# Performance work log

Hardware: AMD Instinct MI355X
Metric: run time of the kernel (lower is better)

Reference implementation:

```python
import jax, jax.numpy as jnp
import numpy as np

B, S, D, H, E, K = 4, 2048, 1024, 4096, 8, 2


def setup_inputs() -> dict:
    key = jax.random.key(0)
    ks = jax.random.split(key, 8)
    scale = 0.02
    x = jax.random.normal(ks[0], (B, S, D), dtype=jnp.float32)
    gate_w = jax.random.normal(ks[1], (D, E), dtype=jnp.float32) * scale
    gate_b = jnp.zeros((E,), dtype=jnp.float32)
    w1 = jax.random.normal(ks[2], (E, D, H), dtype=jnp.float32) * scale
    b1 = jnp.zeros((E, H), dtype=jnp.float32)
    w2 = jax.random.normal(ks[3], (E, H, D), dtype=jnp.float32) * scale
    b2 = jnp.zeros((E, D), dtype=jnp.float32)
    return {"x": x, "gate_w": gate_w, "gate_b": gate_b,
            "w1": w1, "b1": b1, "w2": w2, "b2": b2}


def reference(x, gate_w, gate_b, w1, b1, w2, b2):
    b, s, d = x.shape
    xf = x.reshape(-1, d)                              # [T, D]
    T = xf.shape[0]
    gates = xf @ gate_w + gate_b                       # [T, E]
    scores, idx = jax.lax.top_k(gates, K)              # [T, K] each
    g = jax.nn.softmax(scores, axis=-1)                # softmax over top-k slots
    # Per-token, per-expert combine weight (top-k indices are distinct)
    Wte = jnp.zeros((T, E), dtype=xf.dtype).at[jnp.arange(T)[:, None], idx].add(g)
    # Loop over the small fixed expert set via scan, accumulating weighted outputs.
    def body(acc, p):
        w1e, b1e, w2e, b2e, we = p                     # we: [T]
        h = jax.nn.gelu(xf @ w1e + b1e, approximate=False)  # [T, H]
        y = h @ w2e + b2e                              # [T, D]
        return acc + we[:, None] * y, None
    out, _ = jax.lax.scan(body, jnp.zeros_like(xf), (w1, b1, w2, b2, Wte.T))
    return out.reshape(b, s, d)
```

## Files before the change

kernel.cpp:

```cpp
#include <hip/hip_runtime.h>
#include <hip/hip_bf16.h>

#define Bb 4
#define Ss 2048
#define Dd 1024
#define Hh 4096
#define Ee 8
#define Tt (Bb*Ss)

typedef __attribute__((ext_vector_type(8))) short short8;
typedef __attribute__((ext_vector_type(4))) float floatx4;
typedef unsigned short u16;
typedef unsigned int u32;

__device__ __forceinline__ u16 f2bf(float f) {
  union { float f; u32 u; } v; v.f = f;
  return (u16)((v.u + 0x7FFFu + ((v.u >> 16) & 1u)) >> 16);
}

__device__ __forceinline__ void async16(const u16* g, u16* l) {
  __builtin_amdgcn_global_load_lds(
      (const __attribute__((address_space(1))) unsigned int*)g,
      (__attribute__((address_space(3))) unsigned int*)l, 16, 0, 0);
}

__global__ __launch_bounds__(256) void cvt_x(const float* __restrict__ x, u16* __restrict__ xb) {
  size_t i = ((size_t)blockIdx.x * 256 + threadIdx.x) * 8;
  float4 a = *(const float4*)(x + i);
  float4 b = *(const float4*)(x + i + 4);
  union { u16 us[8]; uint4 v; } o;
  o.us[0] = f2bf(a.x); o.us[1] = f2bf(a.y); o.us[2] = f2bf(a.z); o.us[3] = f2bf(a.w);
  o.us[4] = f2bf(b.x); o.us[5] = f2bf(b.y); o.us[6] = f2bf(b.z); o.us[7] = f2bf(b.w);
  *(uint4*)(xb + i) = o.v;
}

__global__ __launch_bounds__(256) void tconv(const float* __restrict__ src, u16* __restrict__ dst,
                                             int R, int C) {
  __shared__ float tile[64][65];
  int e = blockIdx.z;
  int r0 = blockIdx.y * 64, c0 = blockIdx.x * 64;
  int tx = threadIdx.x & 63, ty = threadIdx.x >> 6;
  const float* s = src + (size_t)e * R * C;
  u16* d = dst + (size_t)e * R * C;
#pragma unroll
  for (int i = 0; i < 16; i++) {
    int r = i * 4 + ty;
    tile[r][tx] = s[(size_t)(r0 + r) * C + c0 + tx];
  }
  __syncthreads();
#pragma unroll
  for (int i = 0; i < 16; i++) {
    int c = i * 4 + ty;
    d[(size_t)(c0 + c) * R + r0 + tx] = f2bf(tile[tx][c]);
  }
}

__global__ __launch_bounds__(256) void gate_kernel(const float* __restrict__ x,
                                                   const float* __restrict__ gw,
                                                   const float* __restrict__ gb,
                                                   int* __restrict__ counts,
                                                   int* __restrict__ tokL,
                                                   int* __restrict__ pairL,
                                                   float* __restrict__ wtL) {
  __shared__ float gwl[Dd * Ee];
  for (int i = threadIdx.x; i < Dd * Ee; i += 256) gwl[i] = gw[i];
  __syncthreads();
  int wid = threadIdx.x >> 6, lane = threadIdx.x & 63;
  int t = blockIdx.x * 4 + wid;
  const float* xr = x + (size_t)t * Dd;
  double acc[Ee];
#pragma unroll
  for (int e = 0; e < Ee; e++) acc[e] = 0.0;
  for (int i = 0; i < Dd / 64; i++) {
    int d = lane + i * 64;
    float xv = xr[d];
#pragma unroll
    for (int e = 0; e < Ee; e++) acc[e] += (double)xv * (double)gwl[d * Ee + e];
  }
#pragma unroll
  for (int off = 32; off > 0; off >>= 1)
#pragma unroll
    for (int e = 0; e < Ee; e++) acc[e] += __shfl_down(acc[e], off);
  if (lane == 0) {
    float s[Ee];
#pragma unroll
    for (int e = 0; e < Ee; e++) s[e] = (float)acc[e] + gb[e];
    int i0 = 0;
#pragma unroll
    for (int e = 1; e < Ee; e++) if (s[e] > s[i0]) i0 = e;
    int i1 = (i0 == 0) ? 1 : 0;
#pragma unroll
    for (int e = 0; e < Ee; e++) if (e != i0 && s[e] > s[i1]) i1 = e;
    float ex = expf(s[i1] - s[i0]);
    float g0 = 1.0f / (1.0f + ex);
    float g1 = ex / (1.0f + ex);
    int p0 = atomicAdd(&counts[i0], 1);
    tokL[i0 * Tt + p0] = t; pairL[i0 * Tt + p0] = t * 2;     wtL[i0 * Tt + p0] = g0;
    int p1 = atomicAdd(&counts[i1], 1);
    tokL[i1 * Tt + p1] = t; pairL[i1 * Tt + p1] = t * 2 + 1; wtL[i1 * Tt + p1] = g1;
  }
}

__global__ __launch_bounds__(256) void gemm1(const u16* __restrict__ xb,
                                             const u16* __restrict__ w1t,
                                             const float* __restrict__ b1,
                                             const int* __restrict__ counts,
                                             const int* __restrict__ tokL,
                                             const int* __restrict__ pairL,
                                             u16* __restrict__ h) {
  const int NT = 32;
  int e = blockIdx.z;
  int cnt = counts[e];
  int flat = blockIdx.x + NT * blockIdx.y;
  int x8 = flat & 7, j = flat >> 3;
  int n_t = j % NT;
  int m_t = (j / NT) * 8 + x8;
  int m0 = m_t * 128;
  if (m0 >= cnt) return;
  int rows = cnt - m0; if (rows > 128) rows = 128;
  int n0 = n_t * 128;

  __shared__ __align__(16) u16 As[2 * 128 * 32];
  __shared__ __align__(16) u16 Bs[2 * 128 * 32];
  __shared__ int ltok[128];
  __shared__ int lpair[128];

  int tid = threadIdx.x;
  if (tid < 128) {
    int ok = tid < rows;
    ltok[tid]  = ok ? tokL[e * Tt + m0 + tid] : tokL[e * Tt + m0];
    lpair[tid] = ok ? pairL[e * Tt + m0 + tid] : 0;
  }
  __syncthreads();

  int wv = tid >> 6, ln = tid & 63;
  int half = wv & 1;
  const u16* gp[4];
  u16* ldst[4];
  if (wv < 2) {
#pragma unroll
    for (int q = 0; q < 4; q++) {
      int r = half * 64 + q * 16 + (ln >> 2);
      int c = (ln & 3) ^ ((r >> 1) & 3);
      gp[q] = xb + (size_t)ltok[r] * Dd + c * 8;
      ldst[q] = As + (half * 64 + q * 16) * 32;
    }
  } else {
#pragma unroll
    for (int q = 0; q < 4; q++) {
      int r = half * 64 + q * 16 + (ln >> 2);
      int c = (ln & 3) ^ ((r >> 1) & 3);
      gp[q] = w1t + ((size_t)e * Hh + n0 + r) * Dd + c * 8;
      ldst[q] = Bs + (half * 64 + q * 16) * 32;
    }
  }

  floatx4 zero4 = {0.f, 0.f, 0.f, 0.f};
  floatx4 acc[4][4];
#pragma unroll
  for (int i = 0; i < 4; i++)
#pragma unroll
    for (int jj = 0; jj < 4; jj++) acc[i][jj] = zero4;

  int wr = wv >> 1, wc = wv & 1;
  int lm = ln & 15, lq = ln >> 4;

  const int NK = Dd / 32;
#pragma unroll
  for (int q = 0; q < 4; q++) async16(gp[q], ldst[q]);
#pragma unroll
  for (int q = 0; q < 4; q++) gp[q] += 32;

  for (int it = 0; it < NK; ++it) {
    if (it + 1 < NK) {
      int nb = (it + 1) & 1;
#pragma unroll
      for (int q = 0; q < 4; q++) async16(gp[q], ldst[q] + nb * 4096);
#pragma unroll
      for (int q = 0; q < 4; q++) gp[q] += 32;
      asm volatile("s_waitcnt vmcnt(4)" ::: "memory");
    } else {
      asm volatile("s_waitcnt vmcnt(0)" ::: "memory");
    }
    __builtin_amdgcn_s_barrier();
    int cb = it & 1;
    const u16* Ab = As + cb * 4096;
    const u16* Bp = Bs + cb * 4096;
    short8 a[4], b[4];
#pragma unroll
    for (int i = 0; i < 4; i++) {
      int row = wr * 64 + i * 16 + lm;
      int p = lq ^ ((row >> 1) & 3);
      a[i] = *(const short8*)(Ab + row * 32 + p * 8);
    }
#pragma unroll
    for (int jj = 0; jj < 4; jj++) {
      int row = wc * 64 + jj * 16 + lm;
      int p = lq ^ ((row >> 1) & 3);
      b[jj] = *(const short8*)(Bp + row * 32 + p * 8);
    }
#pragma unroll
    for (int i = 0; i < 4; i++)
#pragma unroll
      for (int jj = 0; jj < 4; jj++)
        acc[i][jj] = __builtin_amdgcn_mfma_f32_16x16x32_bf16(a[i], b[jj], acc[i][jj], 0, 0, 0);
    asm volatile("s_waitcnt lgkmcnt(0)" ::: "memory");
    __builtin_amdgcn_s_barrier();
  }

#pragma unroll
  for (int i = 0; i < 4; i++) {
    int rbase = wr * 64 + i * 16 + lq * 4;
#pragma unroll
    for (int r = 0; r < 4; r++) {
      int row = rbase + r;
      if (row < rows) {
        int p = lpair[row];
#pragma unroll
        for (int jj = 0; jj < 4; jj++) {
          int col = n0 + wc * 64 + jj * 16 + lm;
          float v = acc[i][jj][r] + b1[e * Hh + col];
          v = 0.5f * v * (1.0f + erff(v * 0.70710678118f));
          h[(size_t)p * Hh + col] = f2bf(v);
        }
      }
    }
  }
}

__global__ __launch_bounds__(256) void gemm2(const u16* __restrict__ h,
                                             const u16* __restrict__ w2t,
                                             const float* __restrict__ b2,
                                             const int* __restrict__ counts,
                                             const int* __restrict__ tokL,
                                             const int* __restrict__ pairL,
                                             const float* __restrict__ wtL,
                                             float* __restrict__ out) {
  const int NT = 8;
  int e = blockIdx.z;
  int cnt = counts[e];
  int flat = blockIdx.x + NT * blockIdx.y;
  int x8 = flat & 7, j = flat >> 3;
  int n_t = j % NT;
  int m_t = (j / NT) * 8 + x8;
  int m0 = m_t * 128;
  if (m0 >= cnt) return;
  int rows = cnt - m0; if (rows > 128) rows = 128;
  int n0 = n_t * 128;

  __shared__ __align__(16) u16 As[2 * 128 * 32];
  __shared__ __align__(16) u16 Bs[2 * 128 * 32];
  __shared__ int ltok[128];
  __shared__ int lpair[128];
  __shared__ float lwt[128];

  int tid = threadIdx.x;
  if (tid < 128) {
    int ok = tid < rows;
    ltok[tid]  = ok ? tokL[e * Tt + m0 + tid] : 0;
    lpair[tid] = ok ? pairL[e * Tt + m0 + tid] : pairL[e * Tt + m0];
    lwt[tid]   = ok ? wtL[e * Tt + m0 + tid] : 0.f;
  }
  __syncthreads();

  int wv = tid >> 6, ln = tid & 63;
  int half = wv & 1;
  const u16* gp[4];
  u16* ldst[4];
  if (wv < 2) {
#pragma unroll
    for (int q = 0; q < 4; q++) {
      int r = half * 64 + q * 16 + (ln >> 2);
      int c = (ln & 3) ^ ((r >> 1) & 3);
      gp[q] = h + (size_t)lpair[r] * Hh + c * 8;
      ldst[q] = As + (half * 64 + q * 16) * 32;
    }
  } else {
#pragma unroll
    for (int q = 0; q < 4; q++) {
      int r = half * 64 + q * 16 + (ln >> 2);
      int c = (ln & 3) ^ ((r >> 1) & 3);
      gp[q] = w2t + ((size_t)e * Dd + n0 + r) * Hh + c * 8;
      ldst[q] = Bs + (half * 64 + q * 16) * 32;
    }
  }

  floatx4 zero4 = {0.f, 0.f, 0.f, 0.f};
  floatx4 acc[4][4];
#pragma unroll
  for (int i = 0; i < 4; i++)
#pragma unroll
    for (int jj = 0; jj < 4; jj++) acc[i][jj] = zero4;

  int wr = wv >> 1, wc = wv & 1;
  int lm = ln & 15, lq = ln >> 4;

  const int NK = Hh / 32;
#pragma unroll
  for (int q = 0; q < 4; q++) async16(gp[q], ldst[q]);
#pragma unroll
  for (int q = 0; q < 4; q++) gp[q] += 32;

  for (int it = 0; it < NK; ++it) {
    if (it + 1 < NK) {
      int nb = (it + 1) & 1;
#pragma unroll
      for (int q = 0; q < 4; q++) async16(gp[q], ldst[q] + nb * 4096);
#pragma unroll
      for (int q = 0; q < 4; q++) gp[q] += 32;
      asm volatile("s_waitcnt vmcnt(4)" ::: "memory");
    } else {
      asm volatile("s_waitcnt vmcnt(0)" ::: "memory");
    }
    __builtin_amdgcn_s_barrier();
    int cb = it & 1;
    const u16* Ab = As + cb * 4096;
    const u16* Bp = Bs + cb * 4096;
    short8 a[4], b[4];
#pragma unroll
    for (int i = 0; i < 4; i++) {
      int row = wr * 64 + i * 16 + lm;
      int p = lq ^ ((row >> 1) & 3);
      a[i] = *(const short8*)(Ab + row * 32 + p * 8);
    }
#pragma unroll
    for (int jj = 0; jj < 4; jj++) {
      int row = wc * 64 + jj * 16 + lm;
      int p = lq ^ ((row >> 1) & 3);
      b[jj] = *(const short8*)(Bp + row * 32 + p * 8);
    }
#pragma unroll
    for (int i = 0; i < 4; i++)
#pragma unroll
      for (int jj = 0; jj < 4; jj++)
        acc[i][jj] = __builtin_amdgcn_mfma_f32_16x16x32_bf16(a[i], b[jj], acc[i][jj], 0, 0, 0);
    asm volatile("s_waitcnt lgkmcnt(0)" ::: "memory");
    __builtin_amdgcn_s_barrier();
  }

#pragma unroll
  for (int i = 0; i < 4; i++) {
    int rbase = wr * 64 + i * 16 + lq * 4;
#pragma unroll
    for (int r = 0; r < 4; r++) {
      int row = rbase + r;
      if (row < rows) {
        int t = ltok[row];
        float w = lwt[row];
#pragma unroll
        for (int jj = 0; jj < 4; jj++) {
          int col = n0 + wc * 64 + jj * 16 + lm;
          float v = (acc[i][jj][r] + b2[e * Dd + col]) * w;
          atomicAdd(out + (size_t)t * Dd + col, v);
        }
      }
    }
  }
}

extern "C" void kernel_launch(void* const* d_in, const int* in_sizes, int n_in,
                              void* d_out, int out_size, void* d_ws, size_t ws_size,
                              hipStream_t stream) {
  const float* x      = (const float*)d_in[0];
  const float* gate_w = (const float*)d_in[1];
  const float* gate_b = (const float*)d_in[2];
  const float* w1     = (const float*)d_in[3];
  const float* b1     = (const float*)d_in[4];
  const float* w2     = (const float*)d_in[5];
  const float* b2     = (const float*)d_in[6];
  float* out = (float*)d_out;

  char* ws = (char*)d_ws;
  size_t off = 0;
  int* counts = (int*)(ws + off); off += 256;
  int* tokL   = (int*)(ws + off); off += (size_t)Ee * Tt * 4;
  int* pairL  = (int*)(ws + off); off += (size_t)Ee * Tt * 4;
  float* wtL  = (float*)(ws + off); off += (size_t)Ee * Tt * 4;
  u16* xb     = (u16*)(ws + off); off += (size_t)Tt * Dd * 2;
  u16* w1t    = (u16*)(ws + off); off += (size_t)Ee * Hh * Dd * 2;
  u16* w2t    = (u16*)(ws + off); off += (size_t)Ee * Dd * Hh * 2;
  u16* hbuf   = (u16*)(ws + off); off += (size_t)Tt * 2 * Hh * 2;

  hipMemsetAsync(counts, 0, 256, stream);
  hipMemsetAsync(out, 0, (size_t)Tt * Dd * 4, stream);

  cvt_x<<<(Tt * Dd) / (256 * 8), 256, 0, stream>>>(x, xb);
  tconv<<<dim3(Hh / 64, Dd / 64, Ee), 256, 0, stream>>>(w1, w1t, Dd, Hh);
  tconv<<<dim3(Dd / 64, Hh / 64, Ee), 256, 0, stream>>>(w2, w2t, Hh, Dd);
  gate_kernel<<<Tt / 4, 256, 0, stream>>>(x, gate_w, gate_b, counts, tokL, pairL, wtL);
  gemm1<<<dim3(32, 64, Ee), 256, 0, stream>>>(xb, w1t, b1, counts, tokL, pairL, hbuf);
  gemm2<<<dim3(8, 64, Ee), 256, 0, stream>>>(hbuf, w2t, b2, counts, tokL, pairL, wtL, out);
}
```

Baseline: 1.110 ms.

## Enlarge grouped GEMM tiles to 256x256, split-K gemm2, and use polynomial GELU

Both expert GEMMs move from 128x128 tiles with 256 threads to 256x256 tiles with 512 threads (8 waves, each computing 128x64), doubling LDS buffers. This raises arithmetic intensity and cuts global/LDS traffic per FLOP. gemm2 also splits K into two halves across blockIdx.z so the grid keeps enough blocks, at the cost of twice as many atomic adds into the output. The exact erff in the GELU epilogue is replaced by the Abramowitz-Stegun polynomial erf approximation with __expf, which adds a small approximation error.

```diff
diff --git a/kernel.cpp b/kernel.cpp
--- a/kernel.cpp
+++ b/kernel.cpp
@@ -16,6 +16,16 @@
 __device__ __forceinline__ u16 f2bf(float f) {
   union { float f; u32 u; } v; v.f = f;
   return (u16)((v.u + 0x7FFFu + ((v.u >> 16) & 1u)) >> 16);
+}
+
+__device__ __forceinline__ float gelu_f(float v) {
+  float z = fabsf(v) * 0.70710678118f;
+  float t = 1.0f / (1.0f + 0.3275911f * z);
+  float p = t * (0.254829592f + t * (-0.284496736f + t * (1.421413741f +
+            t * (-1.453152027f + t * 1.061405429f))));
+  float er = 1.0f - p * __expf(-z * z);
+  er = copysignf(er, v);
+  return 0.5f * v * (1.0f + er);
 }
 
 __device__ __forceinline__ void async16(const u16* g, u16* l) {
@@ -101,32 +111,31 @@
   }
 }
 
-__global__ __launch_bounds__(256) void gemm1(const u16* __restrict__ xb,
-                                             const u16* __restrict__ w1t,
-                                             const float* __restrict__ b1,
-                                             const int* __restrict__ counts,
-                                             const int* __restrict__ tokL,
-                                             const int* __restrict__ pairL,
-                                             u16* __restrict__ h) {
-  const int NT = 32;
+__global__ __launch_bounds__(512, 2) void gemm1(const u16* __restrict__ xb,
+                                                const u16* __restrict__ w1t,
+                                                const float* __restrict__ b1,
+                                                const int* __restrict__ counts,
+                                                const int* __restrict__ tokL,
+                                                const int* __restrict__ pairL,
+                                                u16* __restrict__ h) {
   int e = blockIdx.z;
   int cnt = counts[e];
-  int flat = blockIdx.x + NT * blockIdx.y;
+  int flat = blockIdx.x + 16 * blockIdx.y;
   int x8 = flat & 7, j = flat >> 3;
-  int n_t = j % NT;
-  int m_t = (j / NT) * 8 + x8;
-  int m0 = m_t * 128;
+  int n_t = j & 15;
+  int m_t = (j >> 4) * 8 + x8;
+  int m0 = m_t * 256;
   if (m0 >= cnt) return;
-  int rows = cnt - m0; if (rows > 128) rows = 128;
-  int n0 = n_t * 128;
-
-  __shared__ __align__(16) u16 As[2 * 128 * 32];
-  __shared__ __align__(16) u16 Bs[2 * 128 * 32];
-  __shared__ int ltok[128];
-  __shared__ int lpair[128];
+  int rows = cnt - m0; if (rows > 256) rows = 256;
+  int n0 = n_t * 256;
+
+  __shared__ __align__(16) u16 As[2 * 256 * 32];
+  __shared__ __align__(16) u16 Bs[2 * 256 * 32];
+  __shared__ int ltok[256];
+  __shared__ int lpair[256];
 
   int tid = threadIdx.x;
-  if (tid < 128) {
+  if (tid < 256) {
     int ok = tid < rows;
     ltok[tid]  = ok ? tokL[e * Tt + m0 + tid] : tokL[e * Tt + m0];
     lpair[tid] = ok ? pairL[e * Tt + m0 + tid] : 0;
@@ -134,35 +143,32 @@
   __syncthreads();
 
   int wv = tid >> 6, ln = tid & 63;
-  int half = wv & 1;
   const u16* gp[4];
   u16* ldst[4];
-  if (wv < 2) {
+  {
+    int rbase = (wv & 3) * 64;
 #pragma unroll
     for (int q = 0; q < 4; q++) {
-      int r = half * 64 + q * 16 + (ln >> 2);
+      int r = rbase + q * 16 + (ln >> 2);
       int c = (ln & 3) ^ ((r >> 1) & 3);
-      gp[q] = xb + (size_t)ltok[r] * Dd + c * 8;
-      ldst[q] = As + (half * 64 + q * 16) * 32;
-    }
-  } else {
-#pragma unroll
-    for (int q = 0; q < 4; q++) {
-      int r = half * 64 + q * 16 + (ln >> 2);
-      int c = (ln & 3) ^ ((r >> 1) & 3);
-      gp[q] = w1t + ((size_t)e * Hh + n0 + r) * Dd + c * 8;
-      ldst[q] = Bs + (half * 64 + q * 16) * 32;
+      if (wv < 4) {
+        gp[q] = xb + (size_t)ltok[r] * Dd + c * 8;
+        ldst[q] = As + (rbase + q * 16) * 32;
+      } else {
+        gp[q] = w1t + ((size_t)e * Hh + n0 + r) * Dd + c * 8;
+        ldst[q] = Bs + (rbase + q * 16) * 32;
+      }
     }
   }
 
   floatx4 zero4 = {0.f, 0.f, 0.f, 0.f};
-  floatx4 acc[4][4];
-#pragma unroll
-  for (int i = 0; i < 4; i++)
+  floatx4 acc[8][4];
+#pragma unroll
+  for (int i = 0; i < 8; i++)
 #pragma unroll
     for (int jj = 0; jj < 4; jj++) acc[i][jj] = zero4;
 
-  int wr = wv >> 1, wc = wv & 1;
+  int wr = wv >> 2, wc = wv & 3;
   int lm = ln & 15, lq = ln >> 4;
 
   const int NK = Dd / 32;
@@ -175,7 +181,7 @@
     if (it + 1 < NK) {
       int nb = (it + 1) & 1;
 #pragma unroll
-      for (int q = 0; q < 4; q++) async16(gp[q], ldst[q] + nb * 4096);
+      for (int q = 0; q < 4; q++) async16(gp[q], ldst[q] + nb * 8192);
 #pragma unroll
       for (int q = 0; q < 4; q++) gp[q] += 32;
       asm volatile("s_waitcnt vmcnt(4)" ::: "memory");
@@ -184,12 +190,12 @@
     }
     __builtin_amdgcn_s_barrier();
     int cb = it & 1;
-    const u16* Ab = As + cb * 4096;
-    const u16* Bp = Bs + cb * 4096;
-    short8 a[4], b[4];
-#pragma unroll
-    for (int i = 0; i < 4; i++) {
-      int row = wr * 64 + i * 16 + lm;
+    const u16* Ab = As + cb * 8192;
+    const u16* Bp = Bs + cb * 8192;
+    short8 a[8], b[4];
+#pragma unroll
+    for (int i = 0; i < 8; i++) {
+      int row = wr * 128 + i * 16 + lm;
       int p = lq ^ ((row >> 1) & 3);
       a[i] = *(const short8*)(Ab + row * 32 + p * 8);
     }
@@ -200,7 +206,7 @@
       b[jj] = *(const short8*)(Bp + row * 32 + p * 8);
     }
 #pragma unroll
-    for (int i = 0; i < 4; i++)
+    for (int i = 0; i < 8; i++)
 #pragma unroll
       for (int jj = 0; jj < 4; jj++)
         acc[i][jj] = __builtin_amdgcn_mfma_f32_16x16x32_bf16(a[i], b[jj], acc[i][jj], 0, 0, 0);
@@ -209,8 +215,8 @@
   }
 
 #pragma unroll
-  for (int i = 0; i < 4; i++) {
-    int rbase = wr * 64 + i * 16 + lq * 4;
+  for (int i = 0; i < 8; i++) {
+    int rbase = wr * 128 + i * 16 + lq * 4;
 #pragma unroll
     for (int r = 0; r < 4; r++) {
       int row = rbase + r;
@@ -220,42 +226,42 @@
         for (int jj = 0; jj < 4; jj++) {
           int col = n0 + wc * 64 + jj * 16 + lm;
           float v = acc[i][jj][r] + b1[e * Hh + col];
-          v = 0.5f * v * (1.0f + erff(v * 0.70710678118f));
-          h[(size_t)p * Hh + col] = f2bf(v);
+          h[(size_t)p * Hh + col] = f2bf(gelu_f(v));
         }
       }
     }
   }
 }
 
-__global__ __launch_bounds__(256) void gemm2(const u16* __restrict__ h,
-                                             const u16* __restrict__ w2t,
-                                             const float* __restrict__ b2,
-                                             const int* __restrict__ counts,
-                                             const int* __restrict__ tokL,
-                                             const int* __restrict__ pairL,
-                                             const float* __restrict__ wtL,
-                                             float* __restrict__ out) {
-  const int NT = 8;
-  int e = blockIdx.z;
+__global__ __launch_bounds__(512, 2) void gemm2(const u16* __restrict__ h,
+                                                const u16* __restrict__ w2t,
+                                                const float* __restrict__ b2,
+                                                const int* __restrict__ counts,
+                                                const int* __restrict__ tokL,
+                                                const int* __restrict__ pairL,
+                                                const float* __restrict__ wtL,
+                                                float* __restrict__ out) {
+  int e = blockIdx.z >> 1;
+  int kc = blockIdx.z & 1;
   int cnt = counts[e];
-  int flat = blockIdx.x + NT * blockIdx.y;
+  int flat = blockIdx.x + 4 * blockIdx.y;
   int x8 = flat & 7, j = flat >> 3;
-  int n_t = j % NT;
-  int m_t = (j / NT) * 8 + x8;
-  int m0 = m_t * 128;
+  int n_t = j & 3;
+  int m_t = (j >> 2) * 8 + x8;
+  int m0 = m_t * 256;
   if (m0 >= cnt) return;
-  int rows = cnt - m0; if (rows > 128) rows = 128;
-  int n0 = n_t * 128;
-
-  __shared__ __align__(16) u16 As[2 * 128 * 32];
-  __shared__ __align__(16) u16 Bs[2 * 128 * 32];
-  __shared__ int ltok[128];
-  __shared__ int lpair[128];
-  __shared__ float lwt[128];
+  int rows = cnt - m0; if (rows > 256) rows = 256;
+  int n0 = n_t * 256;
+  int kbase = kc * (Hh / 2);
+
+  __shared__ __align__(16) u16 As[2 * 256 * 32];
+  __shared__ __align__(16) u16 Bs[2 * 256 * 32];
+  __shared__ int ltok[256];
+  __shared__ int lpair[256];
+  __shared__ float lwt[256];
 
   int tid = threadIdx.x;
-  if (tid < 128) {
+  if (tid < 256) {
     int ok = tid < rows;
     ltok[tid]  = ok ? tokL[e * Tt + m0 + tid] : 0;
     lpair[tid] = ok ? pairL[e * Tt + m0 + tid] : pairL[e * Tt + m0];
@@ -264,38 +270,35 @@
   __syncthreads();
 
   int wv = tid >> 6, ln = tid & 63;
-  int half = wv & 1;
   const u16* gp[4];
   u16* ldst[4];
-  if (wv < 2) {
+  {
+    int rbase = (wv & 3) * 64;
 #pragma unroll
     for (int q = 0; q < 4; q++) {
-      int r = half * 64 + q * 16 + (ln >> 2);
+      int r = rbase + q * 16 + (ln >> 2);
       int c = (ln & 3) ^ ((r >> 1) & 3);
-      gp[q] = h + (size_t)lpair[r] * Hh + c * 8;
-      ldst[q] = As + (half * 64 + q * 16) * 32;
-    }
-  } else {
-#pragma unroll
-    for (int q = 0; q < 4; q++) {
-      int r = half * 64 + q * 16 + (ln >> 2);
-      int c = (ln & 3) ^ ((r >> 1) & 3);
-      gp[q] = w2t + ((size_t)e * Dd + n0 + r) * Hh + c * 8;
-      ldst[q] = Bs + (half * 64 + q * 16) * 32;
+      if (wv < 4) {
+        gp[q] = h + (size_t)lpair[r] * Hh + kbase + c * 8;
+        ldst[q] = As + (rbase + q * 16) * 32;
+      } else {
+        gp[q] = w2t + ((size_t)e * Dd + n0 + r) * Hh + kbase + c * 8;
+        ldst[q] = Bs + (rbase + q * 16) * 32;
+      }
     }
   }
 
   floatx4 zero4 = {0.f, 0.f, 0.f, 0.f};
-  floatx4 acc[4][4];
-#pragma unroll
-  for (int i = 0; i < 4; i++)
+  floatx4 acc[8][4];
+#pragma unroll
+  for (int i = 0; i < 8; i++)
 #pragma unroll
     for (int jj = 0; jj < 4; jj++) acc[i][jj] = zero4;
 
-  int wr = wv >> 1, wc = wv & 1;
+  int wr = wv >> 2, wc = wv & 3;
   int lm = ln & 15, lq = ln >> 4;
 
-  const int NK = Hh / 32;
+  const int NK = (Hh / 2) / 32;
 #pragma unroll
   for (int q = 0; q < 4; q++) async16(gp[q], ldst[q]);
 #pragma unroll
@@ -305,7 +308,7 @@
     if (it + 1 < NK) {
       int nb = (it + 1) & 1;
 #pragma unroll
-      for (int q = 0; q < 4; q++) async16(gp[q], ldst[q] + nb * 4096);
+      for (int q = 0; q < 4; q++) async16(gp[q], ldst[q] + nb * 8192);
 #pragma unroll
       for (int q = 0; q < 4; q++) gp[q] += 32;
       asm volatile("s_waitcnt vmcnt(4)" ::: "memory");
@@ -314,12 +317,12 @@
     }
     __builtin_amdgcn_s_barrier();
     int cb = it & 1;
-    const u16* Ab = As + cb * 4096;
-    const u16* Bp = Bs + cb * 4096;
-    short8 a[4], b[4];
-#pragma unroll
-    for (int i = 0; i < 4; i++) {
-      int row = wr * 64 + i * 16 + lm;
+    const u16* Ab = As + cb * 8192;
+    const u16* Bp = Bs + cb * 8192;
+    short8 a[8], b[4];
+#pragma unroll
+    for (int i = 0; i < 8; i++) {
+      int row = wr * 128 + i * 16 + lm;
       int p = lq ^ ((row >> 1) & 3);
       a[i] = *(const short8*)(Ab + row * 32 + p * 8);
     }
@@ -330,7 +333,7 @@
       b[jj] = *(const short8*)(Bp + row * 32 + p * 8);
     }
 #pragma unroll
-    for (int i = 0; i < 4; i++)
+    for (int i = 0; i < 8; i++)
 #pragma unroll
       for (int jj = 0; jj < 4; jj++)
         acc[i][jj] = __builtin_amdgcn_mfma_f32_16x16x32_bf16(a[i], b[jj], acc[i][jj], 0, 0, 0);
@@ -339,8 +342,8 @@
   }
 
 #pragma unroll
-  for (int i = 0; i < 4; i++) {
-    int rbase = wr * 64 + i * 16 + lq * 4;
+  for (int i = 0; i < 8; i++) {
+    int rbase = wr * 128 + i * 16 + lq * 4;
 #pragma unroll
     for (int r = 0; r < 4; r++) {
       int row = rbase + r;
@@ -350,8 +353,8 @@
 #pragma unroll
         for (int jj = 0; jj < 4; jj++) {
           int col = n0 + wc * 64 + jj * 16 + lm;
-          float v = (acc[i][jj][r] + b2[e * Dd + col]) * w;
-          atomicAdd(out + (size_t)t * Dd + col, v);
+          float v = acc[i][jj][r] + (kc == 0 ? b2[e * Dd + col] : 0.f);
+          atomicAdd(out + (size_t)t * Dd + col, v * w);
         }
       }
     }
@@ -388,6 +391,6 @@
   tconv<<<dim3(Hh / 64, Dd / 64, Ee), 256, 0, stream>>>(w1, w1t, Dd, Hh);
   tconv<<<dim3(Dd / 64, Hh / 64, Ee), 256, 0, stream>>>(w2, w2t, Hh, Dd);
   gate_kernel<<<Tt / 4, 256, 0, stream>>>(x, gate_w, gate_b, counts, tokL, pairL, wtL);
-  gemm1<<<dim3(32, 64, Ee), 256, 0, stream>>>(xb, w1t, b1, counts, tokL, pairL, hbuf);
-  gemm2<<<dim3(8, 64, Ee), 256, 0, stream>>>(hbuf, w2t, b2, counts, tokL, pairL, wtL, out);
-}
+  gemm1<<<dim3(16, 32, Ee), 512, 0, stream>>>(xb, w1t, b1, counts, tokL, pairL, hbuf);
+  gemm2<<<dim3(4, 32, 2 * Ee), 512, 0, stream>>>(hbuf, w2t, b2, counts, tokL, pairL, wtL, out);
+}
```

Measured after the change: 1.149 ms. 3.5% more time.
